# Kernel tuning notes

Hardware: AMD Instinct MI355X
Metric: run time of the kernel (lower is better)

## Reference

```python
import jax, jax.numpy as jnp
import numpy as np

ALPHA, GAMMA, EPS = 0.25, 2.0, 1e-8


def _safe_div(num, den):
    # tf.math.divide_no_nan semantics
    return jnp.where(den > 0, num / jnp.where(den > 0, den, 1.0), 0.0)


def giou_loss(b1, b2):
    """tfa.losses.giou_loss: boxes [ymin, xmin, ymax, xmax], broadcastable
    leading dims; returns 1 - GIoU."""
    b1_ymin, b1_xmin, b1_ymax, b1_xmax = jnp.split(b1, 4, axis=-1)
    b2_ymin, b2_xmin, b2_ymax, b2_xmax = jnp.split(b2, 4, axis=-1)
    b1_area = jnp.maximum(b1_ymax - b1_ymin, 0.0) * jnp.maximum(b1_xmax - b1_xmin, 0.0)
    b2_area = jnp.maximum(b2_ymax - b2_ymin, 0.0) * jnp.maximum(b2_xmax - b2_xmin, 0.0)
    i_ymin = jnp.maximum(b1_ymin, b2_ymin)
    i_xmin = jnp.maximum(b1_xmin, b2_xmin)
    i_ymax = jnp.minimum(b1_ymax, b2_ymax)
    i_xmax = jnp.minimum(b1_xmax, b2_xmax)
    inter = jnp.maximum(i_ymax - i_ymin, 0.0) * jnp.maximum(i_xmax - i_xmin, 0.0)
    union = b1_area + b2_area - inter
    iou = _safe_div(inter, union)
    e_ymin = jnp.minimum(b1_ymin, b2_ymin)
    e_xmin = jnp.minimum(b1_xmin, b2_xmin)
    e_ymax = jnp.maximum(b1_ymax, b2_ymax)
    e_xmax = jnp.maximum(b1_xmax, b2_xmax)
    enclose = jnp.maximum(e_ymax - e_ymin, 0.0) * jnp.maximum(e_xmax - e_xmin, 0.0)
    giou = iou - _safe_div(enclose - union, enclose)
    return (1.0 - giou)[..., 0]  # squeeze the split-kept last dim


def setup_inputs() -> dict:
    key = jax.random.key(0)
    k1, k2, k3, k4 = jax.random.split(key, 4)
    b, n, C, m = 8, 16384, 80, 100
    return {
        "cls_pred": jax.random.uniform(k1, (b, n, C), dtype=jnp.float32),
        "loc_pred": jax.random.uniform(k2, (b, n, 4), dtype=jnp.float32),
        "cls_true": jax.random.randint(k3, (b, m, C), 0, 2, dtype=jnp.int32),
        "loc_true": jax.random.uniform(k4, (b, m, 4), dtype=jnp.float32),
        "reg_mask": jnp.ones((b, m), dtype=jnp.float32),
    }


def reference(cls_pred, loc_pred, cls_true, loc_true, reg_mask):
    b, n, C = cls_pred.shape
    m = cls_true.shape[1]
    ct = (cls_true == 1).astype(jnp.float32)  # (b, m, C)

    # focal-style per-(anchor, class) cost; depends only on cls_pred, so
    # contract against the one-hot target with an einsum instead of
    # materializing a (b, m, n, C) tensor.
    p = cls_pred
    neg_cost = (1.0 - ALPHA) * p ** GAMMA * (-jnp.log(1.0 - p + EPS))
    pos_cost = ALPHA * (1.0 - p) ** GAMMA * (-jnp.log(p + EPS))
    cls_loss = jnp.einsum("bnc,bmc->bmn", pos_cost - neg_cost, ct)  # (b, m, n)

    lt = loc_true[:, :, None, :]  # (b, m, 1, 4)
    lp = loc_pred[:, None, :, :]  # (b, 1, n, 4)
    reg_loss = jnp.sum(jnp.abs(lt - lp), axis=-1)  # (b, m, n)
    giou = giou_loss(lp, lt)  # (b, m, n)

    total = 2.0 * cls_loss + 5.0 * reg_loss + 2.0 * giou
    argmin_total = jnp.argmin(total, axis=-1).astype(jnp.int32)  # (b, m)
    batch = jnp.broadcast_to(jnp.arange(b, dtype=jnp.int32)[:, None], (b, m))
    cls_id = jnp.argmax(ct, axis=-1).astype(jnp.int32)
    return jnp.stack([batch, argmin_total, cls_id], axis=-1)  # (b, m, 3)
```

## Files before the change

kernel.cpp:

```cpp
#include <hip/hip_runtime.h>

constexpr int B = 8, N = 16384, C = 80, M = 100;
constexpr int NT = 64;
constexpr int THREADS = 256;
constexpr int NBLK = N / NT;
constexpr int GBLK = NBLK / 2;
constexpr int NFRAG = 21 * 64;

typedef _Float16 half8 __attribute__((ext_vector_type(8)));
typedef float f32x4 __attribute__((ext_vector_type(4)));
typedef unsigned long long u64;

constexpr size_t WS_FT   = 0;
constexpr size_t WS_CID  = 172032;
constexpr size_t WS_WRED = 175232;

__device__ __forceinline__ unsigned ford(float f) {
    unsigned u = __float_as_uint(f);
    return (u & 0x80000000u) ? ~u : (u | 0x80000000u);
}

__device__ __forceinline__ float rcpf(float x) { return __builtin_amdgcn_rcpf(x); }

__device__ __forceinline__ float pair_total(float cls,
    float4 p, float4 t, float a1, float a2,
    float hp, float wp, float ht, float wt)
{
    float ih = fminf(p.z, t.z) - fmaxf(p.x, t.x);
    float iw = fminf(p.w, t.w) - fmaxf(p.y, t.y);
    float inter = fmaxf(ih, 0.f) * fmaxf(iw, 0.f);
    float uni = a1 + a2 - inter;
    float iou = inter * rcpf(fmaxf(uni, 1e-30f));
    float eh = hp + ht - ih;
    float ew = wp + wt - iw;
    float enc = fmaxf(eh, 0.f) * fmaxf(ew, 0.f);
    float ue = (enc - uni) * rcpf(fmaxf(enc, 1e-30f));
    float rg = fabsf(t.x - p.x) + fabsf(t.y - p.y) +
               fabsf(t.z - p.z) + fabsf(t.w - p.w);
    return fmaf(2.5f, rg, cls) + (ue - iou);
}

__device__ __forceinline__ void make_frags(float4 v0, float4 v1,
                                           half8* ah, half8* al)
{
    float pv[8] = { v0.x, v0.y, v0.z, v0.w, v1.x, v1.y, v1.z, v1.w };
    half8 hh, ll;
    #pragma unroll
    for (int j = 0; j < 8; ++j) {
        float p = pv[j], q = 1.0f - p;
        float pos = 0.17328680f * q * q * (-__log2f(p + 1e-8f));
        float neg = 0.51986040f * p * p * (-__log2f(q + 1e-8f));
        float d = pos - neg;
        _Float16 h = (_Float16)d;
        _Float16 r = (_Float16)((d - (float)h) * 2048.0f);
        hh[j] = h;
        ll[j] = r;
    }
    *ah = hh;
    *al = ll;
}

__global__ void prep_light(const int* __restrict__ cls_true,
                           uint4* __restrict__ ftab,
                           int* __restrict__ clsid)
{
    int wid = (blockIdx.x * blockDim.x + threadIdx.x) >> 6;
    int l = threadIdx.x & 63;
    if (wid < B * 21) {
        int b = wid / 21, rem = wid % 21, ch = rem / 7, mf = rem % 7;
        int m = mf * 16 + (l & 15);
        int c0 = ch * 32 + (l >> 4) * 8;
        unsigned w[4] = {0, 0, 0, 0};
        if (m < M) {
            const int* row = cls_true + ((size_t)b * M + m) * C;
            #pragma unroll
            for (int e = 0; e < 8; ++e) {
                int c = c0 + e;
                unsigned h = (c < C && row[c] == 1) ? 0x3C00u : 0u;
                w[e >> 1] |= h << ((e & 1) * 16);
            }
        }
        ftab[(size_t)wid * 64 + l] = make_uint4(w[0], w[1], w[2], w[3]);
    } else if (wid < B * 21 + B * M) {
        int id = wid - B * 21;
        const int* row = cls_true + (size_t)id * C;
        bool v1 = (row[l] == 1);
        bool v2 = (l < 16) ? (row[64 + l] == 1) : false;
        u64 m01 = __ballot(v1);
        u64 m2  = __ballot(v2);
        if (l == 0) {
            int cid = 0;
            if (m01) cid = __ffsll(m01) - 1;
            else if (m2) cid = 64 + __ffsll(m2) - 1;
            clsid[id] = cid;
        }
    }
}

__device__ __forceinline__ void epilogue_tile(
    const f32x4* acc, const float* __restrict__ loc_pred,
    const float* __restrict__ loc_true, u64 (*s_red)[112],
    u64* __restrict__ wred, int b, int n0, int nw, int l, int wv, int t,
    int slot)
{
    const int nbase = n0 + nw + (l >> 4) * 4;
    float4 bx[4];
    float a1[4], hp[4], wp[4];
    #pragma unroll
    for (int r = 0; r < 4; ++r) {
        float4 v = ((const float4*)loc_pred)[(size_t)b * N + nbase + r];
        bx[r] = v;
        hp[r] = v.z - v.x;
        wp[r] = v.w - v.y;
        a1[r] = fmaxf(hp[r], 0.f) * fmaxf(wp[r], 0.f);
    }

    #pragma unroll
    for (int mf = 0; mf < 7; ++mf) {
        int m = mf * 16 + (l & 15);
        int mm = (m < M) ? m : (M - 1);
        float4 tb = ((const float4*)loc_true)[(size_t)b * M + mm];
        float ht = tb.z - tb.x, wt = tb.w - tb.y;
        float a2 = fmaxf(ht, 0.f) * fmaxf(wt, 0.f);
        float tot[4];
        #pragma unroll
        for (int r = 0; r < 4; ++r)
            tot[r] = pair_total(acc[mf][r], bx[r], tb, a1[r], a2,
                                hp[r], wp[r], ht, wt);
        float v = tot[0];
        unsigned ni = (unsigned)nbase;
        #pragma unroll
        for (int r = 1; r < 4; ++r) {
            bool c = tot[r] < v;
            v = c ? tot[r] : v;
            ni = c ? (unsigned)(nbase + r) : ni;
        }
        u64 key = ((u64)ford(v) << 32) | ni;
        #pragma unroll
        for (int off = 16; off <= 32; off <<= 1) {
            u64 o = __shfl_xor(key, off, 64);
            key = (o < key) ? o : key;
        }
        if (l < 16) s_red[wv][m] = key;
    }
    __syncthreads();

    if (t < 112) {
        u64 v0 = s_red[0][t], v1 = s_red[1][t];
        u64 v2 = s_red[2][t], v3 = s_red[3][t];
        u64 a = v0 < v1 ? v0 : v1;
        u64 c = v2 < v3 ? v2 : v3;
        a = a < c ? a : c;
        wred[((size_t)b * NBLK + slot) * 112 + t] = a;
    }
}

__global__ __launch_bounds__(THREADS, 4)
void match_kernel(const float* __restrict__ cls_pred,
                  const float* __restrict__ loc_pred,
                  const uint4* __restrict__ ftab,
                  const float* __restrict__ loc_true,
                  u64* __restrict__ wred)
{
    __shared__ uint4 s_ft[NFRAG];
    __shared__ u64 s_red[4][112];

    const int b  = blockIdx.y;
    const int t  = threadIdx.x;
    const int l  = t & 63;
    const int wv = t >> 6;
    const int nw = wv * 16;

    const float* cpb = cls_pred + (size_t)b * N * 80;
    const int n0a = (blockIdx.x * 2) * NT;
    const int n0b = n0a + NT;

    const int arow0 = n0a + nw + (l & 15);
    float4 av0[3], av1[3];
    #pragma unroll
    for (int kc = 0; kc < 3; ++kc) {
        const int cbase = kc * 32 + (l >> 4) * 8;
        if (cbase < 80) {
            av0[kc] = *(const float4*)&cpb[(size_t)arow0 * 80 + cbase];
            av1[kc] = *(const float4*)&cpb[(size_t)arow0 * 80 + cbase + 4];
        }
    }

    const uint4* ftb = ftab + (size_t)b * NFRAG;
    for (int i = t; i < NFRAG; i += THREADS) s_ft[i] = ftb[i];
    __syncthreads();

    {
        f32x4 acc[7];
        #pragma unroll
        for (int mf = 0; mf < 7; ++mf) acc[mf] = f32x4{0.f, 0.f, 0.f, 0.f};

        #pragma unroll
        for (int kc = 0; kc < 3; ++kc) {
            const int cbase = kc * 32 + (l >> 4) * 8;
            half8 ah = {0,0,0,0,0,0,0,0}, al = {0,0,0,0,0,0,0,0};
            if (cbase < 80) make_frags(av0[kc], av1[kc], &ah, &al);
            #pragma unroll
            for (int mf = 0; mf < 7; ++mf) {
                union { uint4 u; half8 h; } b1, b2;
                b1.u = s_ft[(kc * 7 + mf) * 64 + l];
                b2.u = make_uint4(b1.u.x & 0x10001000u, b1.u.y & 0x10001000u,
                                  b1.u.z & 0x10001000u, b1.u.w & 0x10001000u);
                acc[mf] = __builtin_amdgcn_mfma_f32_16x16x32_f16(ah, b1.h, acc[mf], 0, 0, 0);
                acc[mf] = __builtin_amdgcn_mfma_f32_16x16x32_f16(al, b2.h, acc[mf], 0, 0, 0);
            }
        }
        epilogue_tile(acc, loc_pred, loc_true, s_red, wred,
                      b, n0a, nw, l, wv, t, blockIdx.x * 2);
    }
    __syncthreads();

    {
        const int arow = n0b + nw + (l & 15);
        f32x4 acc[7];
        #pragma unroll
        for (int mf = 0; mf < 7; ++mf) acc[mf] = f32x4{0.f, 0.f, 0.f, 0.f};

        #pragma unroll
        for (int kc = 0; kc < 3; ++kc) {
            const int cbase = kc * 32 + (l >> 4) * 8;
            half8 ah = {0,0,0,0,0,0,0,0}, al = {0,0,0,0,0,0,0,0};
            if (cbase < 80) {
                float4 v0 = *(const float4*)&cpb[(size_t)arow * 80 + cbase];
                float4 v1 = *(const float4*)&cpb[(size_t)arow * 80 + cbase + 4];
                make_frags(v0, v1, &ah, &al);
            }
            #pragma unroll
            for (int mf = 0; mf < 7; ++mf) {
                union { uint4 u; half8 h; } b1, b2;
                b1.u = s_ft[(kc * 7 + mf) * 64 + l];
                b2.u = make_uint4(b1.u.x & 0x10001000u, b1.u.y & 0x10001000u,
                                  b1.u.z & 0x10001000u, b1.u.w & 0x10001000u);
                acc[mf] = __builtin_amdgcn_mfma_f32_16x16x32_f16(ah, b1.h, acc[mf], 0, 0, 0);
                acc[mf] = __builtin_amdgcn_mfma_f32_16x16x32_f16(al, b2.h, acc[mf], 0, 0, 0);
            }
        }
        epilogue_tile(acc, loc_pred, loc_true, s_red, wred,
                      b, n0b, nw, l, wv, t, blockIdx.x * 2 + 1);
    }
}

__global__ __launch_bounds__(256)
void reduce_kernel(const u64* __restrict__ wred,
                   const int* __restrict__ clsid,
                   int* __restrict__ out)
{
    __shared__ u64 s_part[4];
    const int bm = blockIdx.x;
    const int b = bm / M, m = bm % M;
    const int t = threadIdx.x, l = t & 63, wv = t >> 6;

    u64 best = wred[((size_t)b * NBLK + t) * 112 + m];
    #pragma unroll
    for (int off = 1; off < 64; off <<= 1) {
        u64 o = __shfl_xor(best, off, 64);
        best = (o < best) ? o : best;
    }
    if (l == 0) s_part[wv] = best;
    __syncthreads();
    if (t == 0) {
        u64 a0 = s_part[0], a1 = s_part[1];
        u64 a2 = s_part[2], a3 = s_part[3];
        u64 a = a0 < a1 ? a0 : a1;
        u64 c = a2 < a3 ? a2 : a3;
        a = a < c ? a : c;
        out[bm * 3 + 0] = b;
        out[bm * 3 + 1] = (int)(unsigned)(a & 0xFFFFFFFFull);
        out[bm * 3 + 2] = clsid[bm];
    }
}

extern "C" void kernel_launch(void* const* d_in, const int* in_sizes, int n_in,
                              void* d_out, int out_size, void* d_ws, size_t ws_size,
                              hipStream_t stream)
{
    const float* cls_pred = (const float*)d_in[0];
    const float* loc_pred = (const float*)d_in[1];
    const int*   cls_true = (const int*)d_in[2];
    const float* loc_true = (const float*)d_in[3];

    char* ws = (char*)d_ws;
    uint4* ftab  = (uint4*)(ws + WS_FT);
    int*   clsid = (int*)(ws + WS_CID);
    u64*   wred  = (u64*)(ws + WS_WRED);
    int* out = (int*)d_out;

    int prep_waves = B * 21 + B * M;
    prep_light<<<(prep_waves * 64 + 255) / 256, 256, 0, stream>>>(
        cls_true, ftab, clsid);

    dim3 grid(GBLK, B);
    match_kernel<<<grid, THREADS, 0, stream>>>(
        cls_pred, loc_pred, ftab, loc_true, wred);

    reduce_kernel<<<B * M, 256, 0, stream>>>(wred, clsid, out);
}
```

Before: 46.46 us.

## Replace partial-min buffer and reduce kernel with 64-bit atomicMin

Each match block now merges its two tile minima in registers and does a 64-bit atomicMin into a per-(batch, target) packed key, which the prep kernel initialises. The heavy reduce kernel over per-block partials becomes a tiny output kernel that unpacks the winning index. This removes the partial-minimum buffer writes and the cross-block reduction pass. In exchange there is atomic contention from 128 blocks per batch on 100 addresses each.

```diff
diff --git a/kernel.cpp b/kernel.cpp
--- a/kernel.cpp
+++ b/kernel.cpp
@@ -13,7 +13,7 @@
 
 constexpr size_t WS_FT   = 0;
 constexpr size_t WS_CID  = 172032;
-constexpr size_t WS_WRED = 175232;
+constexpr size_t WS_PACK = 175232;
 
 __device__ __forceinline__ unsigned ford(float f) {
     unsigned u = __float_as_uint(f);
@@ -62,7 +62,8 @@
 
 __global__ void prep_light(const int* __restrict__ cls_true,
                            uint4* __restrict__ ftab,
-                           int* __restrict__ clsid)
+                           int* __restrict__ clsid,
+                           u64* __restrict__ packed)
 {
     int wid = (blockIdx.x * blockDim.x + threadIdx.x) >> 6;
     int l = threadIdx.x & 63;
@@ -93,15 +94,15 @@
             if (m01) cid = __ffsll(m01) - 1;
             else if (m2) cid = 64 + __ffsll(m2) - 1;
             clsid[id] = cid;
-        }
-    }
-}
-
-__device__ __forceinline__ void epilogue_tile(
+            packed[id] = 0xFFFFFFFFFFFFFFFFull;
+        }
+    }
+}
+
+__device__ __forceinline__ u64 epilogue_tile(
     const f32x4* acc, const float* __restrict__ loc_pred,
     const float* __restrict__ loc_true, u64 (*s_red)[112],
-    u64* __restrict__ wred, int b, int n0, int nw, int l, int wv, int t,
-    int slot)
+    int b, int n0, int nw, int l, int wv, int t)
 {
     const int nbase = n0 + nw + (l >> 4) * 4;
     float4 bx[4];
@@ -145,14 +146,15 @@
     }
     __syncthreads();
 
+    u64 a = 0xFFFFFFFFFFFFFFFFull;
     if (t < 112) {
         u64 v0 = s_red[0][t], v1 = s_red[1][t];
         u64 v2 = s_red[2][t], v3 = s_red[3][t];
-        u64 a = v0 < v1 ? v0 : v1;
+        a = v0 < v1 ? v0 : v1;
         u64 c = v2 < v3 ? v2 : v3;
         a = a < c ? a : c;
-        wred[((size_t)b * NBLK + slot) * 112 + t] = a;
-    }
+    }
+    return a;
 }
 
 __global__ __launch_bounds__(THREADS, 4)
@@ -160,7 +162,7 @@
                   const float* __restrict__ loc_pred,
                   const uint4* __restrict__ ftab,
                   const float* __restrict__ loc_true,
-                  u64* __restrict__ wred)
+                  u64* __restrict__ packed)
 {
     __shared__ uint4 s_ft[NFRAG];
     __shared__ u64 s_red[4][112];
@@ -190,6 +192,7 @@
     for (int i = t; i < NFRAG; i += THREADS) s_ft[i] = ftb[i];
     __syncthreads();
 
+    u64 best0;
     {
         f32x4 acc[7];
         #pragma unroll
@@ -210,8 +213,8 @@
                 acc[mf] = __builtin_amdgcn_mfma_f32_16x16x32_f16(al, b2.h, acc[mf], 0, 0, 0);
             }
         }
-        epilogue_tile(acc, loc_pred, loc_true, s_red, wred,
-                      b, n0a, nw, l, wv, t, blockIdx.x * 2);
+        best0 = epilogue_tile(acc, loc_pred, loc_true, s_red,
+                              b, n0a, nw, l, wv, t);
     }
     __syncthreads();
 
@@ -240,39 +243,23 @@
                 acc[mf] = __builtin_amdgcn_mfma_f32_16x16x32_f16(al, b2.h, acc[mf], 0, 0, 0);
             }
         }
-        epilogue_tile(acc, loc_pred, loc_true, s_red, wred,
-                      b, n0b, nw, l, wv, t, blockIdx.x * 2 + 1);
-    }
-}
-
-__global__ __launch_bounds__(256)
-void reduce_kernel(const u64* __restrict__ wred,
-                   const int* __restrict__ clsid,
-                   int* __restrict__ out)
-{
-    __shared__ u64 s_part[4];
-    const int bm = blockIdx.x;
-    const int b = bm / M, m = bm % M;
-    const int t = threadIdx.x, l = t & 63, wv = t >> 6;
-
-    u64 best = wred[((size_t)b * NBLK + t) * 112 + m];
-    #pragma unroll
-    for (int off = 1; off < 64; off <<= 1) {
-        u64 o = __shfl_xor(best, off, 64);
-        best = (o < best) ? o : best;
-    }
-    if (l == 0) s_part[wv] = best;
-    __syncthreads();
-    if (t == 0) {
-        u64 a0 = s_part[0], a1 = s_part[1];
-        u64 a2 = s_part[2], a3 = s_part[3];
-        u64 a = a0 < a1 ? a0 : a1;
-        u64 c = a2 < a3 ? a2 : a3;
-        a = a < c ? a : c;
-        out[bm * 3 + 0] = b;
-        out[bm * 3 + 1] = (int)(unsigned)(a & 0xFFFFFFFFull);
-        out[bm * 3 + 2] = clsid[bm];
-    }
+        u64 best1 = epilogue_tile(acc, loc_pred, loc_true, s_red,
+                                  b, n0b, nw, l, wv, t);
+        u64 best = (best0 < best1) ? best0 : best1;
+        if (t < M) atomicMin(&packed[(size_t)b * M + t], best);
+    }
+}
+
+__global__ void out_kernel(const u64* __restrict__ packed,
+                           const int* __restrict__ clsid,
+                           int* __restrict__ out)
+{
+    int idx = blockIdx.x * blockDim.x + threadIdx.x;
+    if (idx >= B * M) return;
+    int b = idx / M;
+    out[idx * 3 + 0] = b;
+    out[idx * 3 + 1] = (int)(unsigned)(packed[idx] & 0xFFFFFFFFull);
+    out[idx * 3 + 2] = clsid[idx];
 }
 
 extern "C" void kernel_launch(void* const* d_in, const int* in_sizes, int n_in,
@@ -287,16 +274,16 @@
     char* ws = (char*)d_ws;
     uint4* ftab  = (uint4*)(ws + WS_FT);
     int*   clsid = (int*)(ws + WS_CID);
-    u64*   wred  = (u64*)(ws + WS_WRED);
+    u64*   packed = (u64*)(ws + WS_PACK);
     int* out = (int*)d_out;
 
     int prep_waves = B * 21 + B * M;
     prep_light<<<(prep_waves * 64 + 255) / 256, 256, 0, stream>>>(
-        cls_true, ftab, clsid);
+        cls_true, ftab, clsid, packed);
 
     dim3 grid(GBLK, B);
     match_kernel<<<grid, THREADS, 0, stream>>>(
-        cls_pred, loc_pred, ftab, loc_true, wred);
-
-    reduce_kernel<<<B * M, 256, 0, stream>>>(wred, clsid, out);
-}
+        cls_pred, loc_pred, ftab, loc_true, packed);
+
+    out_kernel<<<(B * M + 255) / 256, 256, 0, stream>>>(packed, clsid, out);
+}
```

Measured after the change: 45.77 us. No clear change (-1.5%).
